# Kernel tuning notes

Measured on AMD Instinct MI355X. Metric: run time of the kernel, lower is better.

The kernel has to match this reference:

```python
import jax, jax.numpy as jnp
import numpy as np

B, N, D, K = 128, 1000, 196, 48
SIGMA = 0.05


def setup_inputs() -> dict:
    key = jax.random.key(0)
    kx, kn = jax.random.split(key)
    x = jax.random.normal(kx, (B, D), dtype=jnp.float32)
    noise = jax.random.normal(kn, (B, N, D), dtype=jnp.float32)
    return {"x": x, "noise": noise, "sigma": SIGMA}


def reference(x, noise, sigma):
    # x: (b, d); noise: (b, n, d)
    b, d = x.shape
    n = noise.shape[1]
    perturbed = x[:, None, :] + noise * sigma          # (b, n, d)
    _, idx = jax.lax.top_k(perturbed, K)               # (b, n, k) indices into d
    idx = jnp.sort(idx, axis=-1)                       # sorted, as in torch code
    # indicators[b,k,d'] = mean_n one_hot(idx[b,n,k])[d']
    # computed via scatter-add, avoiding the (b,n,k,d) one-hot tensor
    b_idx = jnp.arange(b)[:, None, None]               # (b,1,1)
    k_idx = jnp.arange(K)[None, None, :]               # (1,1,k)
    indicators = jnp.zeros((b, K, d), dtype=x.dtype).at[b_idx, k_idx, idx].add(1.0 / n)
    return indicators
```

## Files before the change

### kernel.cpp

```cpp
#include <hip/hip_runtime.h>


#define BB 128
#define NN 1000
#define DD 196
#define KK 48

constexpr int SPLIT   = 8;
constexpr int ROWS    = NN / SPLIT;
constexpr int THREADS = 512;
constexpr int NWAVES  = THREADS / 64;
constexpr int DH      = DD / 2;
constexpr int LDSN    = KK * DH;

__device__ __forceinline__ int mbcnt64(unsigned long long m) {
  return __builtin_amdgcn_mbcnt_hi((unsigned)(m >> 32),
         __builtin_amdgcn_mbcnt_lo((unsigned)m, 0));
}

template <int PAT>
__device__ __forceinline__ float swz(float v) {
  return __int_as_float(__builtin_amdgcn_ds_swizzle(__float_as_int(v), PAT));
}

__device__ __forceinline__ float wave_min_f32(float m) {
  m = fminf(m, swz<0x041F>(m));
  m = fminf(m, swz<0x081F>(m));
  m = fminf(m, swz<0x101F>(m));
  m = fminf(m, swz<0x201F>(m));
  m = fminf(m, swz<0x401F>(m));
  float a = __int_as_float(__builtin_amdgcn_readlane(__float_as_int(m), 0));
  float b = __int_as_float(__builtin_amdgcn_readlane(__float_as_int(m), 32));
  return fminf(a, b);
}
__device__ __forceinline__ float wave_max_f32(float m) {
  m = fmaxf(m, swz<0x041F>(m));
  m = fmaxf(m, swz<0x081F>(m));
  m = fmaxf(m, swz<0x101F>(m));
  m = fmaxf(m, swz<0x201F>(m));
  m = fmaxf(m, swz<0x401F>(m));
  float a = __int_as_float(__builtin_amdgcn_readlane(__float_as_int(m), 0));
  float b = __int_as_float(__builtin_amdgcn_readlane(__float_as_int(m), 32));
  return fmaxf(a, b);
}

__device__ __forceinline__ unsigned key_of(float v) {
  unsigned u = __float_as_uint(v);
  return u ^ (0x80000000u | (unsigned)((int)u >> 31));
}

__global__ __launch_bounds__(64) void pivot_kernel(
    const float* __restrict__ x, float* __restrict__ piv) {
  const int b    = blockIdx.x;
  const int lane = threadIdx.x;
  const bool lv  = lane < 49;
  float4 xv = make_float4(0.f, 0.f, 0.f, 0.f);
  if (lv) xv = *reinterpret_cast<const float4*>(x + b * DD + 4 * lane);
  unsigned xk0 = lv ? key_of(xv.x) : 0u;
  unsigned xk1 = lv ? key_of(xv.y) : 0u;
  unsigned xk2 = lv ? key_of(xv.z) : 0u;
  unsigned xk3 = lv ? key_of(xv.w) : 0u;
  unsigned p = 0u;
  #pragma unroll
  for (int bit = 31; bit >= 0; --bit) {
    unsigned cand = p | (1u << bit);
    int c = __popcll(__ballot(xk0 >= cand)) + __popcll(__ballot(xk1 >= cand))
          + __popcll(__ballot(xk2 >= cand)) + __popcll(__ballot(xk3 >= cand));
    if (c >= KK) p = cand;
  }
  if (lane == 0) {
    unsigned u = (p & 0x80000000u) ? (p ^ 0x80000000u) : ~p;
    piv[b] = __uint_as_float(u);
  }
}

__global__ __launch_bounds__(THREADS) void ptopk_kernel(
    const float* __restrict__ x, const float* __restrict__ noise,
    const float* __restrict__ sigp, const float* __restrict__ pivp,
    float* __restrict__ out) {
  __shared__ unsigned cnt[LDSN];
  const int tid   = threadIdx.x;
  const int b     = blockIdx.x / SPLIT;
  const int split = blockIdx.x % SPLIT;

  for (int i = tid; i < LDSN; i += THREADS) cnt[i] = 0u;
  __syncthreads();

  const float sigma = sigp[0];
  const float piv   = pivp[b];
  const int lane = tid & 63;
  const int wv   = tid >> 6;
  const bool lv  = lane < 49;
  const float PINF = __builtin_huge_valf();
  const float NINF = -__builtin_huge_valf();

  float4 xv = make_float4(0.f, 0.f, 0.f, 0.f);
  if (lv) xv = *reinterpret_cast<const float4*>(x + b * DD + 4 * lane);

  const float* nbase = noise + ((size_t)b * NN + (size_t)split * ROWS) * DD;

  float4 nv = make_float4(0.f, 0.f, 0.f, 0.f);
  if (lv && wv < ROWS)
    nv = *reinterpret_cast<const float4*>(nbase + (size_t)wv * DD + 4 * lane);

  for (int r = wv; r < ROWS; r += NWAVES) {
    const float4 cur = nv;
    if (lv && (r + NWAVES) < ROWS)
      nv = *reinterpret_cast<const float4*>(nbase + (size_t)(r + NWAVES) * DD + 4 * lane);

    const float v0 = lv ? fmaf(sigma, cur.x, xv.x) : NINF;
    const float v1 = lv ? fmaf(sigma, cur.y, xv.y) : NINF;
    const float v2 = lv ? fmaf(sigma, cur.z, xv.z) : NINF;
    const float v3 = lv ? fmaf(sigma, cur.w, xv.w) : NINF;

    bool s0 = v0 > piv, s1 = v1 > piv, s2 = v2 > piv, s3 = v3 > piv;
    unsigned long long S0 = __ballot(s0), S1 = __ballot(s1),
                       S2 = __ballot(s2), S3 = __ballot(s3);
    const int c = __popcll(S0) + __popcll(S1) + __popcll(S2) + __popcll(S3);

    if (c > KK) {
      int need = c - KK;
      float m0 = s0 ? v0 : PINF, m1 = s1 ? v1 : PINF;
      float m2 = s2 ? v2 : PINF, m3 = s3 ? v3 : PINF;
      for (;;) {
        const float mm = wave_min_f32(fminf(fminf(m0, m1), fminf(m2, m3)));
        const bool e0 = (m0 == mm), e1 = (m1 == mm),
                   e2 = (m2 == mm), e3 = (m3 == mm);
        const unsigned long long E0 = __ballot(e0), E1 = __ballot(e1),
                                 E2 = __ballot(e2), E3 = __ballot(e3);
        const int cv = __popcll(E0) + __popcll(E1) + __popcll(E2) + __popcll(E3);
        if (cv <= need) {
          s0 &= !e0; s1 &= !e1; s2 &= !e2; s3 &= !e3;
          need -= cv;
          if (need == 0) break;
          m0 = e0 ? PINF : m0; m1 = e1 ? PINF : m1;
          m2 = e2 ? PINF : m2; m3 = e3 ? PINF : m3;
        } else {
          const int keep = cv - need;
          int tp = mbcnt64(E0) + mbcnt64(E1) + mbcnt64(E2) + mbcnt64(E3);
          if (e0 && tp >= keep) s0 = false;  tp += e0 ? 1 : 0;
          if (e1 && tp >= keep) s1 = false;  tp += e1 ? 1 : 0;
          if (e2 && tp >= keep) s2 = false;  tp += e2 ? 1 : 0;
          if (e3 && tp >= keep) s3 = false;
          break;
        }
      }
      S0 = __ballot(s0); S1 = __ballot(s1); S2 = __ballot(s2); S3 = __ballot(s3);
    } else if (c < KK) {
      int need = KK - c;
      float m0 = s0 ? NINF : v0, m1 = s1 ? NINF : v1;
      float m2 = s2 ? NINF : v2, m3 = s3 ? NINF : v3;
      for (;;) {
        const float mm = wave_max_f32(fmaxf(fmaxf(m0, m1), fmaxf(m2, m3)));
        const bool e0 = (m0 == mm), e1 = (m1 == mm),
                   e2 = (m2 == mm), e3 = (m3 == mm);
        const unsigned long long E0 = __ballot(e0), E1 = __ballot(e1),
                                 E2 = __ballot(e2), E3 = __ballot(e3);
        const int cv = __popcll(E0) + __popcll(E1) + __popcll(E2) + __popcll(E3);
        if (cv <= need) {
          s0 |= e0; s1 |= e1; s2 |= e2; s3 |= e3;
          need -= cv;
          if (need == 0) break;
          m0 = e0 ? NINF : m0; m1 = e1 ? NINF : m1;
          m2 = e2 ? NINF : m2; m3 = e3 ? NINF : m3;
        } else {
          int tp = mbcnt64(E0) + mbcnt64(E1) + mbcnt64(E2) + mbcnt64(E3);
          if (e0 && tp < need) s0 = true;  tp += e0 ? 1 : 0;
          if (e1 && tp < need) s1 = true;  tp += e1 ? 1 : 0;
          if (e2 && tp < need) s2 = true;  tp += e2 ? 1 : 0;
          if (e3 && tp < need) s3 = true;
          break;
        }
      }
      S0 = __ballot(s0); S1 = __ballot(s1); S2 = __ballot(s2); S3 = __ballot(s3);
    }

    int kp = mbcnt64(S0) + mbcnt64(S1) + mbcnt64(S2) + mbcnt64(S3);
    const int b2 = 2 * lane;
    if (s0) atomicAdd(&cnt[kp * DH + b2],     1u);        kp += s0 ? 1 : 0;
    if (s1) atomicAdd(&cnt[kp * DH + b2],     0x10000u);  kp += s1 ? 1 : 0;
    if (s2) atomicAdd(&cnt[kp * DH + b2 + 1], 1u);        kp += s2 ? 1 : 0;
    if (s3) atomicAdd(&cnt[kp * DH + b2 + 1], 0x10000u);
  }

  __syncthreads();

  const float invn = 1.0f / (float)NN;
  float* ob = out + (size_t)b * KK * DD;
  for (int i = tid; i < LDSN; i += THREADS) {
    const unsigned cv = cnt[i];
    if (cv) {
      const int k   = i / DH;
      const int dd2 = i - k * DH;
      const unsigned lo = cv & 0xFFFFu, hi = cv >> 16;
      float* p = ob + k * DD + 2 * dd2;
      if (lo) atomicAdd(p,     (float)lo * invn);
      if (hi) atomicAdd(p + 1, (float)hi * invn);
    }
  }
}

extern "C" void kernel_launch(void* const* d_in, const int* in_sizes, int n_in,
                              void* d_out, int out_size, void* d_ws, size_t ws_size,
                              hipStream_t stream) {
  (void)in_sizes; (void)n_in; (void)ws_size;
  const float* x     = (const float*)d_in[0];
  const float* noise = (const float*)d_in[1];
  const float* sig   = (const float*)d_in[2];
  float* out = (float*)d_out;
  float* piv = (float*)d_ws;

  (void)hipMemsetAsync(d_out, 0, (size_t)out_size * sizeof(float), stream);
  pivot_kernel<<<dim3(BB), dim3(64), 0, stream>>>(x, piv);
  ptopk_kernel<<<dim3(BB * SPLIT), dim3(THREADS), 0, stream>>>(x, noise, sig, piv, out);
}
```

Before: 172.5 us.

## Split rows across more smaller blocks and use DPP wave reductions

Raises the per-batch row split from 8 to 16 blocks with 256 threads each, using uneven row ranges because 1000 is not divisible by 16. This aims to improve occupancy and load balance across CUs. The wave min/max reductions switch from ds_swizzle to DPP row_shr/row_bcast steps with a single readlane. More blocks also means more LDS zeroing and more global atomic flushes per batch.

Result: no change. 170.4 us (-1.2%).

```diff
diff --git a/kernel.cpp b/kernel.cpp
--- a/kernel.cpp
+++ b/kernel.cpp
@@ -6,9 +6,8 @@
 #define DD 196
 #define KK 48
 
-constexpr int SPLIT   = 8;
-constexpr int ROWS    = NN / SPLIT;
-constexpr int THREADS = 512;
+constexpr int SPLIT   = 16;
+constexpr int THREADS = 256;
 constexpr int NWAVES  = THREADS / 64;
 constexpr int DH      = DD / 2;
 constexpr int LDSN    = KK * DH;
@@ -18,30 +17,36 @@
          __builtin_amdgcn_mbcnt_lo((unsigned)m, 0));
 }
 
-template <int PAT>
-__device__ __forceinline__ float swz(float v) {
-  return __int_as_float(__builtin_amdgcn_ds_swizzle(__float_as_int(v), PAT));
+template <int CTRL>
+__device__ __forceinline__ float dpp_min_step(float v) {
+  int t = __builtin_amdgcn_update_dpp(__float_as_int(v), __float_as_int(v),
+                                      CTRL, 0xF, 0xF, false);
+  return fminf(v, __int_as_float(t));
+}
+template <int CTRL>
+__device__ __forceinline__ float dpp_max_step(float v) {
+  int t = __builtin_amdgcn_update_dpp(__float_as_int(v), __float_as_int(v),
+                                      CTRL, 0xF, 0xF, false);
+  return fmaxf(v, __int_as_float(t));
 }
 
 __device__ __forceinline__ float wave_min_f32(float m) {
-  m = fminf(m, swz<0x041F>(m));
-  m = fminf(m, swz<0x081F>(m));
-  m = fminf(m, swz<0x101F>(m));
-  m = fminf(m, swz<0x201F>(m));
-  m = fminf(m, swz<0x401F>(m));
-  float a = __int_as_float(__builtin_amdgcn_readlane(__float_as_int(m), 0));
-  float b = __int_as_float(__builtin_amdgcn_readlane(__float_as_int(m), 32));
-  return fminf(a, b);
+  m = dpp_min_step<0x111>(m);
+  m = dpp_min_step<0x112>(m);
+  m = dpp_min_step<0x114>(m);
+  m = dpp_min_step<0x118>(m);
+  m = dpp_min_step<0x142>(m);
+  m = dpp_min_step<0x143>(m);
+  return __int_as_float(__builtin_amdgcn_readlane(__float_as_int(m), 63));
 }
 __device__ __forceinline__ float wave_max_f32(float m) {
-  m = fmaxf(m, swz<0x041F>(m));
-  m = fmaxf(m, swz<0x081F>(m));
-  m = fmaxf(m, swz<0x101F>(m));
-  m = fmaxf(m, swz<0x201F>(m));
-  m = fmaxf(m, swz<0x401F>(m));
-  float a = __int_as_float(__builtin_amdgcn_readlane(__float_as_int(m), 0));
-  float b = __int_as_float(__builtin_amdgcn_readlane(__float_as_int(m), 32));
-  return fmaxf(a, b);
+  m = dpp_max_step<0x111>(m);
+  m = dpp_max_step<0x112>(m);
+  m = dpp_max_step<0x114>(m);
+  m = dpp_max_step<0x118>(m);
+  m = dpp_max_step<0x142>(m);
+  m = dpp_max_step<0x143>(m);
+  return __int_as_float(__builtin_amdgcn_readlane(__float_as_int(m), 63));
 }
 
 __device__ __forceinline__ unsigned key_of(float v) {
@@ -82,6 +87,8 @@
   const int tid   = threadIdx.x;
   const int b     = blockIdx.x / SPLIT;
   const int split = blockIdx.x % SPLIT;
+  const int n0    = (split * NN) / SPLIT;
+  const int n1    = ((split + 1) * NN) / SPLIT;
 
   for (int i = tid; i < LDSN; i += THREADS) cnt[i] = 0u;
   __syncthreads();
@@ -97,15 +104,15 @@
   float4 xv = make_float4(0.f, 0.f, 0.f, 0.f);
   if (lv) xv = *reinterpret_cast<const float4*>(x + b * DD + 4 * lane);
 
-  const float* nbase = noise + ((size_t)b * NN + (size_t)split * ROWS) * DD;
+  const float* nbase = noise + (size_t)b * NN * DD;
 
   float4 nv = make_float4(0.f, 0.f, 0.f, 0.f);
-  if (lv && wv < ROWS)
-    nv = *reinterpret_cast<const float4*>(nbase + (size_t)wv * DD + 4 * lane);
-
-  for (int r = wv; r < ROWS; r += NWAVES) {
+  if (lv && (n0 + wv) < n1)
+    nv = *reinterpret_cast<const float4*>(nbase + (size_t)(n0 + wv) * DD + 4 * lane);
+
+  for (int r = n0 + wv; r < n1; r += NWAVES) {
     const float4 cur = nv;
-    if (lv && (r + NWAVES) < ROWS)
+    if (lv && (r + NWAVES) < n1)
       nv = *reinterpret_cast<const float4*>(nbase + (size_t)(r + NWAVES) * DD + 4 * lane);
 
     const float v0 = lv ? fmaf(sigma, cur.x, xv.x) : NINF;
```
